# Kernel tuning notes

Measured on AMD Instinct MI355X. Metric: run time of the kernel, lower is better.

The kernel has to match this reference:

```python
import jax, jax.numpy as jnp
import numpy as np
import math

B, T, E, H = 4, 2048, 1024, 16
D = E // H

def setup_inputs() -> dict:
    key = jax.random.key(0)
    k1, k2, k3 = jax.random.split(key, 3)
    x = jax.random.normal(k1, (B, T, E), dtype=jnp.float32)
    # GPT-2 Conv1D: out = x @ W + b, W shape [in, out]
    W_attn = jax.random.normal(k2, (E, 3 * E), dtype=jnp.float32) * 0.02
    b_attn = jnp.zeros((3 * E,), dtype=jnp.float32)
    W_proj = jax.random.normal(k3, (E, E), dtype=jnp.float32) * 0.02
    b_proj = jnp.zeros((E,), dtype=jnp.float32)
    # causal mask, broadcastable [1,1,T,T]; masked where mask == 0
    mask = jnp.tril(jnp.ones((T, T), dtype=jnp.int32))[None, None]
    return {"x": x, "mask": mask, "W_attn": W_attn, "b_attn": b_attn,
            "W_proj": W_proj, "b_proj": b_proj}

def reference(x, mask, W_attn, b_attn, W_proj, b_proj):
    Bx, Tx, Ex = x.shape
    qkv = x @ W_attn + b_attn                      # [B,T,3E]
    q, k, v = jnp.split(qkv, 3, axis=-1)
    q = q.reshape(Bx, Tx, H, D)
    k = k.reshape(Bx, Tx, H, D)
    v = v.reshape(Bx, Tx, H, D)
    att = jnp.einsum('bqhd,bkhd->bhqk', q, k) / math.sqrt(D)
    att = jnp.where(mask == 0, jnp.float32(-1e20), att)
    att = jax.nn.softmax(att, axis=-1)
    y = jnp.einsum('bhqk,bkhd->bqhd', att, v).reshape(Bx, Tx, Ex)
    y = y @ W_proj + b_proj
    return y
```

## Files before the change

### kernel.cpp

```cpp
#include <hip/hip_runtime.h>
#include <hip/hip_bf16.h>

#define BB 4
#define TT 2048
#define EE 1024
#define HH 16
#define DD 64
#define PART_SZ (BB*HH*TT*DD)

typedef __bf16 bf16x8_t __attribute__((ext_vector_type(8)));
typedef float floatx4_t __attribute__((ext_vector_type(4)));

__device__ __forceinline__ unsigned short f2bf(float f) {
    union { float f; unsigned int i; } v; v.f = f;
    unsigned int x = v.i;
    return (unsigned short)((x + 0x7FFFu + ((x >> 16) & 1u)) >> 16);
}
__device__ __forceinline__ unsigned short f2bf_trunc(float f) {
    union { float f; unsigned int i; } v; v.f = f;
    return (unsigned short)(v.i >> 16);
}
__device__ __forceinline__ unsigned int pack2(float lo, float hi) {
    return (unsigned int)f2bf(lo) | ((unsigned int)f2bf(hi) << 16);
}

typedef __attribute__((address_space(1))) const unsigned int gu32_t;
typedef __attribute__((address_space(3))) unsigned int lu32_t;
__device__ __forceinline__ void gl_lds16(const unsigned short* g, unsigned short* l) {
    __builtin_amdgcn_global_load_lds((gu32_t*)g, (lu32_t*)l, 16, 0, 0);
}

template<int CTRL>
__device__ __forceinline__ float dpp_mv(float x) {
    return __int_as_float(__builtin_amdgcn_mov_dpp(__float_as_int(x), CTRL, 0xF, 0xF, true));
}
__device__ __forceinline__ float row16_sum(float x) {
    x += dpp_mv<0xB1>(x);
    x += dpp_mv<0x4E>(x);
    x += dpp_mv<0x141>(x);
    x += dpp_mv<0x140>(x);
    return x;
}

__global__ __launch_bounds__(256)
void cvt_x_k(const float* __restrict__ x, unsigned short* __restrict__ xb)
{
    const size_t i = ((size_t)blockIdx.x * 256 + threadIdx.x) * 8;
    float4 a = *(const float4*)(x + i);
    float4 b = *(const float4*)(x + i + 4);
    uint4 p;
    p.x = pack2(a.x, a.y); p.y = pack2(a.z, a.w);
    p.z = pack2(b.x, b.y); p.w = pack2(b.z, b.w);
    *(uint4*)(xb + i) = p;
}

__global__ __launch_bounds__(256)
void transpose_w_k(const float* __restrict__ W, unsigned short* __restrict__ WT, int N)
{
    __shared__ unsigned short L[64 * 72];
    const int tid = threadIdx.x;
    const int tn = blockIdx.x * 64;
    const int tk = blockIdx.y * 64;
    {
        const int k  = tid >> 2;
        const int n0 = (tid & 3) * 16;
        const float* src = W + (size_t)(tk + k) * N + tn + n0;
        float4 f0 = *(const float4*)(src);
        float4 f1 = *(const float4*)(src + 4);
        float4 f2 = *(const float4*)(src + 8);
        float4 f3 = *(const float4*)(src + 12);
        uint4 p0, p1;
        p0.x = pack2(f0.x, f0.y); p0.y = pack2(f0.z, f0.w);
        p0.z = pack2(f1.x, f1.y); p0.w = pack2(f1.z, f1.w);
        p1.x = pack2(f2.x, f2.y); p1.y = pack2(f2.z, f2.w);
        p1.z = pack2(f3.x, f3.y); p1.w = pack2(f3.z, f3.w);
        *(uint4*)(&L[k * 72 + n0])     = p0;
        *(uint4*)(&L[k * 72 + n0 + 8]) = p1;
    }
    __syncthreads();
    {
        const int n  = tid >> 2;
        const int k0 = (tid & 3) * 16;
        unsigned short u[16];
        #pragma unroll
        for (int e = 0; e < 16; e++) u[e] = L[(k0 + e) * 72 + n];
        unsigned short* dst = WT + (size_t)(tn + n) * 1024 + tk + k0;
        *(uint4*)(dst)     = *(uint4*)&u[0];
        *(uint4*)(dst + 8) = *(uint4*)&u[8];
    }
}

template<int MODE>
__global__ __launch_bounds__(256, 2)
void gemm_k(const unsigned short* __restrict__ Ag,
            const unsigned short* __restrict__ Wt,
            const float* __restrict__ biasg,
            unsigned short* __restrict__ Qo,
            unsigned short* __restrict__ Ko,
            unsigned short* __restrict__ Vo,
            float* __restrict__ Fo)
{
    constexpr int N = (MODE == 0) ? 3072 : 1024;
    __shared__ unsigned short Al[128 * 32];
    __shared__ unsigned short Bl[128 * 32];
    constexpr size_t EPSZ = (MODE == 0) ? (4 * 16 * 72 * 2) : (4 * 16 * 68 * 4);
    __shared__ __align__(16) char EpRaw[EPSZ];
    const int tid  = threadIdx.x;
    int bn, bm;
    if (MODE == 0) {
        const int id = blockIdx.x;
        const int s  = id & 7;
        const int t  = id >> 3;
        const int P  = (t / 12) * 8 + s;
        bm = (P >> 1) * 128;
        bn = ((P & 1) * 12 + (t % 12)) * 128;
    } else {
        const int id = blockIdx.x;
        const int s  = id & 7;
        const int t  = id >> 3;
        bm = ((t & 7) * 8 + s) * 128;
        bn = (t >> 3) * 128;
    }
    const int lane = tid & 63;
    const int wv   = tid >> 6;
    const int wm   = (wv & 1) * 64;
    const int wn   = (wv >> 1) * 64;
    const int l16  = lane & 15;
    const int quad = lane >> 4;
    const int lrow = lane >> 2;
    const int lk   = (lane & 3) * 8;

    const bool flip = (MODE == 1) || (bn < 2 * EE);

    floatx4_t acc[4][4];
    #pragma unroll
    for (int i = 0; i < 4; i++)
        #pragma unroll
        for (int j = 0; j < 4; j++)
            acc[i][j] = (floatx4_t){0.f, 0.f, 0.f, 0.f};

    for (int k0 = 0; k0 < 1024; k0 += 32) {
        __syncthreads();
        #pragma unroll
        for (int t = 0; t < 2; t++) {
            const int rb = wv * 32 + t * 16;
            gl_lds16(Ag + (size_t)(bm + rb + lrow) * 1024 + k0 + lk, &Al[rb * 32]);
            gl_lds16(Wt + (size_t)(bn + rb + lrow) * 1024 + k0 + lk, &Bl[rb * 32]);
        }
        __syncthreads();

        bf16x8_t af[4], bfr[4];
        #pragma unroll
        for (int i = 0; i < 4; i++)
            af[i]  = *(const bf16x8_t*)(&Al[(wm + i * 16 + l16) * 32 + quad * 8]);
        #pragma unroll
        for (int j = 0; j < 4; j++)
            bfr[j] = *(const bf16x8_t*)(&Bl[(wn + j * 16 + l16) * 32 + quad * 8]);
        if (flip) {
            #pragma unroll
            for (int u = 0; u < 4; u++)
                #pragma unroll
                for (int v = 0; v < 4; v++)
                    acc[u][v] = __builtin_amdgcn_mfma_f32_16x16x32_bf16(bfr[u], af[v], acc[u][v], 0, 0, 0);
        } else {
            #pragma unroll
            for (int u = 0; u < 4; u++)
                #pragma unroll
                for (int v = 0; v < 4; v++)
                    acc[u][v] = __builtin_amdgcn_mfma_f32_16x16x32_bf16(af[u], bfr[v], acc[u][v], 0, 0, 0);
        }
    }

    const int rdrow = lane >> 2;
    const int rdseg = (lane & 3) * 16;

    if (MODE == 1) {
        float* Epf = (float*)EpRaw + wv * 16 * 68;
        floatx4_t bv[4];
        #pragma unroll
        for (int u = 0; u < 4; u++)
            bv[u] = *(const floatx4_t*)(biasg + bn + wn + u * 16 + quad * 4);
        #pragma unroll
        for (int v = 0; v < 4; v++) {
            #pragma unroll
            for (int u = 0; u < 4; u++) {
                floatx4_t val;
                #pragma unroll
                for (int rr = 0; rr < 4; rr++) val[rr] = acc[u][v][rr] + bv[u][rr];
                *(floatx4_t*)(&Epf[l16 * 68 + u * 16 + quad * 4]) = val;
            }
            __builtin_amdgcn_s_waitcnt(0);
            const int m = bm + wm + v * 16 + rdrow;
            float* dst = Fo + (size_t)m * N + bn + wn + rdseg;
            const float* srcl = &Epf[rdrow * 68 + rdseg];
            #pragma unroll
            for (int c = 0; c < 4; c++)
                *(floatx4_t*)(dst + c * 4) = *(const floatx4_t*)(srcl + c * 4);
        }
    } else if (flip) {
        unsigned short* Ep = (unsigned short*)EpRaw + wv * 16 * 72;
        floatx4_t bv[4];
        #pragma unroll
        for (int u = 0; u < 4; u++)
            bv[u] = *(const floatx4_t*)(biasg + bn + wn + u * 16 + quad * 4);
        const int p  = bn >> 10;
        const int h  = ((bn + wn) & 1023) >> 6;
        const int d0 = rdseg & 63;
        unsigned short* outb = (p == 0) ? Qo : Ko;
        #pragma unroll
        for (int v = 0; v < 4; v++) {
            #pragma unroll
            for (int u = 0; u < 4; u++) {
                uint2 pk;
                pk.x = pack2(acc[u][v][0] + bv[u][0], acc[u][v][1] + bv[u][1]);
                pk.y = pack2(acc[u][v][2] + bv[u][2], acc[u][v][3] + bv[u][3]);
                *(uint2*)(&Ep[l16 * 72 + u * 16 + quad * 4]) = pk;
            }
            __builtin_amdgcn_s_waitcnt(0);
            const int t  = bm + wm + v * 16 + rdrow;
            const int b_ = t >> 11, t_ = t & 2047;
            unsigned short* dst = outb + ((size_t)(b_ * HH + h) * TT + t_) * DD + d0;
            const unsigned short* srcl = &Ep[rdrow * 72 + rdseg];
            *(uint4*)(dst)     = *(const uint4*)(srcl);
            *(uint4*)(dst + 8) = *(const uint4*)(srcl + 8);
        }
    } else {
        unsigned short* Ep = (unsigned short*)EpRaw + wv * 16 * 72;
        #pragma unroll
        for (int v = 0; v < 4; v++) {
            const float bias_v = biasg[bn + wn + v * 16 + l16];
            #pragma unroll
            for (int u = 0; u < 4; u++) {
                uint2 pk;
                pk.x = pack2(acc[u][v][0] + bias_v, acc[u][v][1] + bias_v);
                pk.y = pack2(acc[u][v][2] + bias_v, acc[u][v][3] + bias_v);
                *(uint2*)(&Ep[l16 * 72 + u * 16 + quad * 4]) = pk;
            }
            __builtin_amdgcn_s_waitcnt(0);
            const int n  = bn + wn + v * 16 + rdrow;
            const int h  = (n & 1023) >> 6, d = n & 63;
            const int t0 = bm + wm + rdseg;
            const int b_ = t0 >> 11, t_ = t0 & 2047;
            unsigned short* dst = Vo + ((size_t)(b_ * HH + h) * DD + d) * TT + t_;
            const unsigned short* srcl = &Ep[rdrow * 72 + rdseg];
            *(uint4*)(dst)     = *(const uint4*)(srcl);
            *(uint4*)(dst + 8) = *(const uint4*)(srcl + 8);
        }
    }
}

__global__ __launch_bounds__(256, 4)
void attn_k(const unsigned short* __restrict__ Qg,
            const unsigned short* __restrict__ Kg,
            const unsigned short* __restrict__ Vg,
            unsigned short* __restrict__ Og)
{
    __shared__ unsigned short Kt[64 * 72];
    __shared__ unsigned short Vt[64 * 72];
    __shared__ unsigned short Pw[4][16 * 72];
    const int tid  = threadIdx.x;
    const int w    = tid >> 6;
    const int lane = tid & 63;
    const int l16  = lane & 15;
    const int quad = lane >> 4;
    const int id = blockIdx.x;
    const int qt = 31 - ((id >> 3) & 31);
    const int bh = (id & 7) + 8 * (id >> 8);
    const int qb   = qt * 64;
    const int qw   = qb + w * 16;
    const size_t base = (size_t)bh * TT * DD;
    const float C = 0.18033688f;

    bf16x8_t qf[2];
    #pragma unroll
    for (int ks = 0; ks < 2; ks++)
        qf[ks] = *(const bf16x8_t*)(Qg + base + (size_t)(qw + l16) * DD + ks * 32 + quad * 8);

    floatx4_t oacc[4];
    #pragma unroll
    for (int n = 0; n < 4; n++) oacc[n] = (floatx4_t){0.f, 0.f, 0.f, 0.f};
    float lacc[4] = {0.f, 0.f, 0.f, 0.f};

    const int kend = qb + 64;
    const int srow = tid >> 2;
    const int sc0  = (tid & 3) * 16;
    for (int kb = 0; kb < kend; kb += 64) {
        __syncthreads();
        {
            const unsigned short* kg = Kg + base + (size_t)(kb + srow) * DD + sc0;
            uint4 ka = *(const uint4*)(kg);
            uint4 kb2 = *(const uint4*)(kg + 8);
            *(uint4*)(&Kt[srow * 72 + sc0])     = ka;
            *(uint4*)(&Kt[srow * 72 + sc0 + 8]) = kb2;
            const unsigned short* vg = Vg + base + (size_t)srow * TT + kb + sc0;
            uint4 va = *(const uint4*)(vg);
            uint4 vb = *(const uint4*)(vg + 8);
            *(uint4*)(&Vt[srow * 72 + sc0])     = va;
            *(uint4*)(&Vt[srow * 72 + sc0 + 8]) = vb;
        }
        __syncthreads();
        if (kb < qw + 16) {
            floatx4_t sacc[4];
            #pragma unroll
            for (int n = 0; n < 4; n++) sacc[n] = (floatx4_t){0.f, 0.f, 0.f, 0.f};
            #pragma unroll
            for (int n = 0; n < 4; n++) {
                #pragma unroll
                for (int ks = 0; ks < 2; ks++) {
                    bf16x8_t kf = *(const bf16x8_t*)(&Kt[(n * 16 + l16) * 72 + ks * 32 + quad * 8]);
                    sacc[n] = __builtin_amdgcn_mfma_f32_16x16x32_bf16(qf[ks], kf, sacc[n], 0, 0, 0);
                }
            }
            if ((kb + 63) > qw) {
                const int q0 = qw + quad * 4;
                #pragma unroll
                for (int n = 0; n < 4; n++) {
                    const int key = kb + n * 16 + l16;
                    #pragma unroll
                    for (int rr = 0; rr < 4; rr++)
                        if (key > q0 + rr) sacc[n][rr] = -1e30f;
                }
            }
            #pragma unroll
            for (int n = 0; n < 4; n++) {
                #pragma unroll
                for (int rr = 0; rr < 4; rr++) {
                    const float p = __builtin_exp2f(sacc[n][rr] * C);
                    sacc[n][rr] = p;
                    lacc[rr] += p;
                    Pw[w][(quad * 4 + rr) * 72 + n * 16 + l16] = f2bf_trunc(p);
                }
            }
            bf16x8_t pf[2];
            #pragma unroll
            for (int ks = 0; ks < 2; ks++)
                pf[ks] = *(const bf16x8_t*)(&Pw[w][l16 * 72 + ks * 32 + quad * 8]);
            #pragma unroll
            for (int n = 0; n < 4; n++) {
                #pragma unroll
                for (int ks = 0; ks < 2; ks++) {
                    bf16x8_t vf = *(const bf16x8_t*)(&Vt[(n * 16 + l16) * 72 + ks * 32 + quad * 8]);
                    oacc[n] = __builtin_amdgcn_mfma_f32_16x16x32_bf16(pf[ks], vf, oacc[n], 0, 0, 0);
                }
            }
        }
    }
    const int b_ = bh >> 4, h_ = bh & 15;
    #pragma unroll
    for (int rr = 0; rr < 4; rr++) {
        const float inv = 1.f / row16_sum(lacc[rr]);
        const int q = qw + quad * 4 + rr;
        unsigned short* op = Og + (((size_t)b_ * TT + q) * HH + h_) * DD;
        #pragma unroll
        for (int n = 0; n < 4; n++)
            op[n * 16 + l16] = f2bf(oacc[n][rr] * inv);
    }
}

extern "C" void kernel_launch(void* const* d_in, const int* in_sizes, int n_in,
                              void* d_out, int out_size, void* d_ws, size_t ws_size,
                              hipStream_t stream) {
    const float* x      = (const float*)d_in[0];
    const float* W_attn = (const float*)d_in[2];
    const float* b_attn = (const float*)d_in[3];
    const float* W_proj = (const float*)d_in[4];
    const float* b_proj = (const float*)d_in[5];
    float* out = (float*)d_out;

    unsigned short* Qs  = (unsigned short*)d_out;
    unsigned short* Ks  = Qs + (size_t)PART_SZ;
    unsigned short* VTs = (unsigned short*)d_ws;
    unsigned short* Ao  = VTs + (size_t)PART_SZ;
    unsigned short* Xb  = Ao + (size_t)PART_SZ;
    unsigned short* WaT = Xb + (size_t)PART_SZ;
    unsigned short* WpT = WaT + (size_t)3072 * 1024;

    cvt_x_k<<<PART_SZ / (256 * 8), 256, 0, stream>>>(x, Xb);
    transpose_w_k<<<dim3(48, 16), 256, 0, stream>>>(W_attn, WaT, 3072);
    transpose_w_k<<<dim3(16, 16), 256, 0, stream>>>(W_proj, WpT, 1024);

    gemm_k<0><<<1536, 256, 0, stream>>>(Xb, WaT, b_attn, Qs, Ks, VTs, nullptr);

    attn_k<<<2048, 256, 0, stream>>>(Qs, Ks, VTs, Ao);

    gemm_k<1><<<512, 256, 0, stream>>>(Ao, WpT, b_proj, nullptr, nullptr, nullptr, out);
}
```

Baseline: 309.0 us.

## Compute transposed S in attention and pass P through registers via bpermute

The attention kernel swaps the MFMA operands so each lane holds scores for one query row across keys. The probabilities are then packed to bf16 with v_cvt_pk_bf16 and rearranged into the A-operand layout with ds_bpermute, replacing the per-wave LDS round trip for P. The row-sum reduction becomes two shuffles, and launch bounds rise from 4 to 6 blocks per SM now that the P buffer no longer uses LDS. This adds bpermute traffic and more register pressure, and P rounding changes from truncation to round-to-nearest.

Result: slower. 351.1 us (+13.6%).

```diff
diff --git a/kernel.cpp b/kernel.cpp
--- a/kernel.cpp
+++ b/kernel.cpp
@@ -16,30 +16,19 @@
     unsigned int x = v.i;
     return (unsigned short)((x + 0x7FFFu + ((x >> 16) & 1u)) >> 16);
 }
-__device__ __forceinline__ unsigned short f2bf_trunc(float f) {
-    union { float f; unsigned int i; } v; v.f = f;
-    return (unsigned short)(v.i >> 16);
-}
 __device__ __forceinline__ unsigned int pack2(float lo, float hi) {
     return (unsigned int)f2bf(lo) | ((unsigned int)f2bf(hi) << 16);
+}
+__device__ __forceinline__ unsigned int cvt_pk_bf16(float lo, float hi) {
+    unsigned int r;
+    asm("v_cvt_pk_bf16_f32 %0, %1, %2" : "=v"(r) : "v"(lo), "v"(hi));
+    return r;
 }
 
 typedef __attribute__((address_space(1))) const unsigned int gu32_t;
 typedef __attribute__((address_space(3))) unsigned int lu32_t;
 __device__ __forceinline__ void gl_lds16(const unsigned short* g, unsigned short* l) {
     __builtin_amdgcn_global_load_lds((gu32_t*)g, (lu32_t*)l, 16, 0, 0);
-}
-
-template<int CTRL>
-__device__ __forceinline__ float dpp_mv(float x) {
-    return __int_as_float(__builtin_amdgcn_mov_dpp(__float_as_int(x), CTRL, 0xF, 0xF, true));
-}
-__device__ __forceinline__ float row16_sum(float x) {
-    x += dpp_mv<0xB1>(x);
-    x += dpp_mv<0x4E>(x);
-    x += dpp_mv<0x141>(x);
-    x += dpp_mv<0x140>(x);
-    return x;
 }
 
 __global__ __launch_bounds__(256)
@@ -249,7 +238,7 @@
     }
 }
 
-__global__ __launch_bounds__(256, 4)
+__global__ __launch_bounds__(256, 6)
 void attn_k(const unsigned short* __restrict__ Qg,
             const unsigned short* __restrict__ Kg,
             const unsigned short* __restrict__ Vg,
@@ -257,7 +246,6 @@
 {
     __shared__ unsigned short Kt[64 * 72];
     __shared__ unsigned short Vt[64 * 72];
-    __shared__ unsigned short Pw[4][16 * 72];
     const int tid  = threadIdx.x;
     const int w    = tid >> 6;
     const int lane = tid & 63;
@@ -279,7 +267,11 @@
     floatx4_t oacc[4];
     #pragma unroll
     for (int n = 0; n < 4; n++) oacc[n] = (floatx4_t){0.f, 0.f, 0.f, 0.f};
-    float lacc[4] = {0.f, 0.f, 0.f, 0.f};
+    float lacc = 0.f;
+
+    const int t0b  = (lane >> 4) & 1;
+    const int idx0 = (l16 + 32 * t0b) * 4;
+    const int idx1 = idx0 + 64;
 
     const int kend = qb + 64;
     const int srow = tid >> 2;
@@ -308,52 +300,62 @@
                 #pragma unroll
                 for (int ks = 0; ks < 2; ks++) {
                     bf16x8_t kf = *(const bf16x8_t*)(&Kt[(n * 16 + l16) * 72 + ks * 32 + quad * 8]);
-                    sacc[n] = __builtin_amdgcn_mfma_f32_16x16x32_bf16(qf[ks], kf, sacc[n], 0, 0, 0);
+                    sacc[n] = __builtin_amdgcn_mfma_f32_16x16x32_bf16(kf, qf[ks], sacc[n], 0, 0, 0);
                 }
             }
             if ((kb + 63) > qw) {
-                const int q0 = qw + quad * 4;
+                const int kq = kb + quad * 4;
+                const int qq = qw + l16;
                 #pragma unroll
                 for (int n = 0; n < 4; n++) {
-                    const int key = kb + n * 16 + l16;
                     #pragma unroll
                     for (int rr = 0; rr < 4; rr++)
-                        if (key > q0 + rr) sacc[n][rr] = -1e30f;
+                        if (kq + n * 16 + rr > qq) sacc[n][rr] = -1e30f;
                 }
             }
+            unsigned int Wp[4][2];
             #pragma unroll
             for (int n = 0; n < 4; n++) {
-                #pragma unroll
-                for (int rr = 0; rr < 4; rr++) {
-                    const float p = __builtin_exp2f(sacc[n][rr] * C);
-                    sacc[n][rr] = p;
-                    lacc[rr] += p;
-                    Pw[w][(quad * 4 + rr) * 72 + n * 16 + l16] = f2bf_trunc(p);
+                const float p0 = __builtin_exp2f(sacc[n][0] * C);
+                const float p1 = __builtin_exp2f(sacc[n][1] * C);
+                const float p2 = __builtin_exp2f(sacc[n][2] * C);
+                const float p3 = __builtin_exp2f(sacc[n][3] * C);
+                lacc += (p0 + p1) + (p2 + p3);
+                Wp[n][0] = cvt_pk_bf16(p0, p1);
+                Wp[n][1] = cvt_pk_bf16(p2, p3);
+            }
+            #pragma unroll
+            for (int ks = 0; ks < 2; ks++) {
+                union { unsigned int u[4]; bf16x8_t v; } pf;
+                #pragma unroll
+                for (int k = 0; k < 4; k++) {
+                    const int idx = (k >> 1) ? idx1 : idx0;
+                    const int a = __builtin_amdgcn_ds_bpermute(idx, (int)Wp[2 * ks][k & 1]);
+                    const int b = __builtin_amdgcn_ds_bpermute(idx, (int)Wp[2 * ks + 1][k & 1]);
+                    pf.u[k] = (unsigned int)((lane & 32) ? b : a);
                 }
-            }
-            bf16x8_t pf[2];
-            #pragma unroll
-            for (int ks = 0; ks < 2; ks++)
-                pf[ks] = *(const bf16x8_t*)(&Pw[w][l16 * 72 + ks * 32 + quad * 8]);
-            #pragma unroll
-            for (int n = 0; n < 4; n++) {
-                #pragma unroll
-                for (int ks = 0; ks < 2; ks++) {
+                #pragma unroll
+                for (int n = 0; n < 4; n++) {
                     bf16x8_t vf = *(const bf16x8_t*)(&Vt[(n * 16 + l16) * 72 + ks * 32 + quad * 8]);
-                    oacc[n] = __builtin_amdgcn_mfma_f32_16x16x32_bf16(pf[ks], vf, oacc[n], 0, 0, 0);
+                    oacc[n] = __builtin_amdgcn_mfma_f32_16x16x32_bf16(pf.v, vf, oacc[n], 0, 0, 0);
                 }
             }
         }
     }
+    float lsum = lacc;
+    lsum += __shfl_xor(lsum, 16);
+    lsum += __shfl_xor(lsum, 32);
+    const float inv = 1.f / lsum;
     const int b_ = bh >> 4, h_ = bh & 15;
     #pragma unroll
     for (int rr = 0; rr < 4; rr++) {
-        const float inv = 1.f / row16_sum(lacc[rr]);
+        const float invr = __int_as_float(
+            __builtin_amdgcn_ds_bpermute((quad * 4 + rr) * 4, __float_as_int(inv)));
         const int q = qw + quad * 4 + rr;
         unsigned short* op = Og + (((size_t)b_ * TT + q) * HH + h_) * DD;
         #pragma unroll
         for (int n = 0; n < 4; n++)
-            op[n * 16 + l16] = f2bf(oacc[n][rr] * inv);
+            op[n * 16 + l16] = f2bf(oacc[n][rr] * invr);
     }
 }
 
```

## Double-buffer K/V tiles in LDS with register prefetch in attention kernel

Applied to the files above, without the earlier changes.

The attention kernel now keeps two LDS buffers for K and V. While computing on one tile, it loads the next tile's global data into registers. This overlaps global-memory latency with MFMA and softmax work, and cuts the barriers per key tile from two to one. In exchange, LDS use per block roughly doubles for K/V and register pressure rises, which may lower occupancy under the 4-blocks-per-CU launch bound.

New measurement: 316.5 us. +2.4%, slower.

```diff
diff --git a/kernel.cpp b/kernel.cpp
--- a/kernel.cpp
+++ b/kernel.cpp
@@ -255,8 +255,8 @@
             const unsigned short* __restrict__ Vg,
             unsigned short* __restrict__ Og)
 {
-    __shared__ unsigned short Kt[64 * 72];
-    __shared__ unsigned short Vt[64 * 72];
+    __shared__ unsigned short Kt[2][64 * 72];
+    __shared__ unsigned short Vt[2][64 * 72];
     __shared__ unsigned short Pw[4][16 * 72];
     const int tid  = threadIdx.x;
     const int w    = tid >> 6;
@@ -281,24 +281,30 @@
     for (int n = 0; n < 4; n++) oacc[n] = (floatx4_t){0.f, 0.f, 0.f, 0.f};
     float lacc[4] = {0.f, 0.f, 0.f, 0.f};
 
-    const int kend = qb + 64;
     const int srow = tid >> 2;
     const int sc0  = (tid & 3) * 16;
-    for (int kb = 0; kb < kend; kb += 64) {
-        __syncthreads();
-        {
-            const unsigned short* kg = Kg + base + (size_t)(kb + srow) * DD + sc0;
-            uint4 ka = *(const uint4*)(kg);
-            uint4 kb2 = *(const uint4*)(kg + 8);
-            *(uint4*)(&Kt[srow * 72 + sc0])     = ka;
-            *(uint4*)(&Kt[srow * 72 + sc0 + 8]) = kb2;
-            const unsigned short* vg = Vg + base + (size_t)srow * TT + kb + sc0;
-            uint4 va = *(const uint4*)(vg);
-            uint4 vb = *(const uint4*)(vg + 8);
-            *(uint4*)(&Vt[srow * 72 + sc0])     = va;
-            *(uint4*)(&Vt[srow * 72 + sc0 + 8]) = vb;
-        }
-        __syncthreads();
+    const unsigned short* kg0 = Kg + base + (size_t)srow * DD + sc0;
+    const unsigned short* vg0 = Vg + base + (size_t)srow * TT + sc0;
+    const int nt = qt + 1;
+
+    uint4 kA0, kA1, vA0, vA1;
+    uint4 kB0, kB1, vB0, vB1;
+
+#define LDSET(TI, K0, K1, V0, V1) do {                                   \
+        const unsigned short* kg = kg0 + (size_t)(TI) * 64 * DD;         \
+        K0 = *(const uint4*)(kg);  K1 = *(const uint4*)(kg + 8);         \
+        const unsigned short* vg = vg0 + (TI) * 64;                      \
+        V0 = *(const uint4*)(vg);  V1 = *(const uint4*)(vg + 8);         \
+    } while (0)
+
+#define STSET(BUF, K0, K1, V0, V1) do {                                  \
+        *(uint4*)(&Kt[BUF][srow * 72 + sc0])     = K0;                   \
+        *(uint4*)(&Kt[BUF][srow * 72 + sc0 + 8]) = K1;                   \
+        *(uint4*)(&Vt[BUF][srow * 72 + sc0])     = V0;                   \
+        *(uint4*)(&Vt[BUF][srow * 72 + sc0 + 8]) = V1;                   \
+    } while (0)
+
+    auto COMP = [&](int kb, int buf) {
         if (kb < qw + 16) {
             floatx4_t sacc[4];
             #pragma unroll
@@ -307,7 +313,7 @@
             for (int n = 0; n < 4; n++) {
                 #pragma unroll
                 for (int ks = 0; ks < 2; ks++) {
-                    bf16x8_t kf = *(const bf16x8_t*)(&Kt[(n * 16 + l16) * 72 + ks * 32 + quad * 8]);
+                    bf16x8_t kf = *(const bf16x8_t*)(&Kt[buf][(n * 16 + l16) * 72 + ks * 32 + quad * 8]);
                     sacc[n] = __builtin_amdgcn_mfma_f32_16x16x32_bf16(qf[ks], kf, sacc[n], 0, 0, 0);
                 }
             }
@@ -339,12 +345,29 @@
             for (int n = 0; n < 4; n++) {
                 #pragma unroll
                 for (int ks = 0; ks < 2; ks++) {
-                    bf16x8_t vf = *(const bf16x8_t*)(&Vt[(n * 16 + l16) * 72 + ks * 32 + quad * 8]);
+                    bf16x8_t vf = *(const bf16x8_t*)(&Vt[buf][(n * 16 + l16) * 72 + ks * 32 + quad * 8]);
                     oacc[n] = __builtin_amdgcn_mfma_f32_16x16x32_bf16(pf[ks], vf, oacc[n], 0, 0, 0);
                 }
             }
         }
-    }
+    };
+
+    LDSET(0, kA0, kA1, vA0, vA1);
+    for (int t = 0; t < nt; t += 2) {
+        STSET(0, kA0, kA1, vA0, vA1);
+        if (t + 1 < nt) LDSET(t + 1, kB0, kB1, vB0, vB1);
+        __syncthreads();
+        COMP(t * 64, 0);
+        if (t + 1 < nt) {
+            STSET(1, kB0, kB1, vB0, vB1);
+            if (t + 2 < nt) LDSET(t + 2, kA0, kA1, vA0, vA1);
+            __syncthreads();
+            COMP((t + 1) * 64, 1);
+        }
+    }
+#undef LDSET
+#undef STSET
+
     const int b_ = bh >> 4, h_ = bh & 15;
     #pragma unroll
     for (int rr = 0; rr < 4; rr++) {
```
